# Optimization experiments

Measured on AMD Instinct MI355X. Metric: run time of the kernel, lower is better.

Reference implementation:

```python
import jax, jax.numpy as jnp
import numpy as np

# Module hyper-parameters (from create_with_implicit_mesh defaults)
KERNEL_RADIUS = 4
KERNEL_SIGMA2 = 0.5
EPS = 1e-8


def _forward_shift(src, flow):
    """Flow-based forward splatting with Gaussian-kernel scatter-add.

    Each source pixel at integer grid location (x, y) lands at the continuous
    target position p = (x + u, y + v). Its value is splatted onto all target
    pixels within KERNEL_RADIUS of p with weight exp(-||t - p||^2 / (2*sigma2)),
    accumulated atomically into weighted-image / weight / mask buffers.
    """
    B, C, H, W = src.shape
    HW = H * W
    R = KERNEL_RADIUS
    dt = src.dtype

    xs = jnp.arange(W, dtype=dt)
    ys = jnp.arange(H, dtype=dt)
    px = (xs[None, None, :] + flow[:, 0]).reshape(B, HW)   # continuous landing x
    py = (ys[None, :, None] + flow[:, 1]).reshape(B, HW)   # continuous landing y
    bx = jnp.floor(px).astype(jnp.int32)                   # base integer target
    by = jnp.floor(py).astype(jnp.int32)

    src_f = src.reshape(B, C, HW)
    acc_wI = jnp.zeros((B, C, HW), dt)
    acc_w = jnp.zeros((B, HW), dt)

    b2 = jnp.arange(B)[:, None]                 # (B,1) for (B,HW) scatter
    b3 = jnp.arange(B)[:, None, None]           # (B,1,1) for (B,C,HW) scatter
    c3 = jnp.arange(C)[None, :, None]           # (1,C,1)

    r2 = jnp.asarray(R * R, dt)
    for dy in range(-R, R + 1):
        for dx in range(-R, R + 1):
            tx = bx + dx
            ty = by + dy
            fx = tx.astype(dt)
            fy = ty.astype(dt)
            d2 = (fx - px) ** 2 + (fy - py) ** 2
            valid = (tx >= 0) & (tx < W) & (ty >= 0) & (ty < H) & (d2 <= r2)
            w = jnp.exp(-d2 / (2.0 * KERNEL_SIGMA2)) * valid.astype(dt)  # (B,HW)
            idx = jnp.clip(ty, 0, H - 1) * W + jnp.clip(tx, 0, W - 1)    # (B,HW)
            acc_w = acc_w.at[b2, idx].add(w)
            acc_wI = acc_wI.at[b3, c3, idx[:, None, :]].add(w[:, None, :] * src_f)

    w_img = acc_w.reshape(B, 1, H, W)
    out_img = acc_wI.reshape(B, C, H, W) / (w_img + EPS)
    mask = (w_img > 0).astype(dt)
    return out_img, mask


def setup_inputs() -> dict:
    key = jax.random.key(0)
    k1, k2 = jax.random.split(key)
    B, C, H, W = 4, 3, 720, 1280
    src_image = jax.random.normal(k1, (B, C, H, W), dtype=jnp.float32)
    flow_src_to_tar = jax.random.normal(k2, (B, 2, H, W), dtype=jnp.float32)
    return {"src_image": src_image, "flow_src_to_tar": flow_src_to_tar}


def reference(src_image, flow_src_to_tar):
    return _forward_shift(src_image, flow_src_to_tar)
```

## Files before the change

kernel.cpp:

```cpp
#include <hip/hip_runtime.h>
#include <hip/hip_fp16.h>

constexpr int B_N = 4;
constexpr int C_N = 3;
constexpr int H_IMG = 720;
constexpr int W_IMG = 1280;
constexpr int HW = H_IMG * W_IMG;

constexpr int TW = 64, TH = 32;
constexpr int HALO = 8;
constexpr int CW = TW + 2 * HALO;
constexpr int CH = TH + 2 * HALO;
constexpr int PITCH = CW + 1;
constexpr int PLANE = CH * PITCH;
constexpr float FLOW_MAX = 4.0f;
constexpr float LOG2E = 1.44269504f;

#define K1 0.36787944117144233f
#define K3 0.049787068367863944f
#define K5 0.006737946999085467f
#define K7 0.0009118819655545162f

typedef float v2f __attribute__((ext_vector_type(2)));
static __device__ __forceinline__ v2f splat2(float x) { return (v2f){x, x}; }

__global__ __launch_bounds__(256, 3)
void gather_kernel(const float* __restrict__ src, const float* __restrict__ flow,
                   float* __restrict__ out) {
    __shared__ __half2 UV[PLANE];
    __shared__ __half2 S01[PLANE];
    __shared__ float   S2[PLANE];

    const int b = blockIdx.z;
    const int tx0 = blockIdx.x * TW;
    const int ty0 = blockIdx.y * TH;
    const int cx0 = tx0 - HALO, cy0 = ty0 - HALO;

    const float* __restrict__ up = flow + (size_t)(b * 2) * HW;
    const float* __restrict__ vp = up + HW;
    const float* __restrict__ sp = src + (size_t)(b * 3) * HW;

    for (int idx = threadIdx.x; idx < CH * CW; idx += 256) {
        const int cy = idx / CW, cx = idx - cy * CW;
        const int gx = cx0 + cx, gy = cy0 + cy;
        float u = 300.f, v = 300.f, s0 = 0.f, s1 = 0.f, s2 = 0.f;
        if (gx >= 0 && gx < W_IMG && gy >= 0 && gy < H_IMG) {
            const int g = gy * W_IMG + gx;
            const float uu = up[g], vv = vp[g];
            if (fabsf(uu) <= FLOW_MAX && fabsf(vv) <= FLOW_MAX) {
                u = uu; v = vv;
                s0 = sp[g]; s1 = sp[HW + g]; s2 = sp[2 * HW + g];
            }
        }
        const int l = cy * PITCH + cx;
        UV[l] = __floats2half2_rn(u, v);
        S01[l] = __floats2half2_rn(s0, s1);
        S2[l] = s2;
    }
    __syncthreads();

    const int xg = threadIdx.x & 7;
    const int rL = threadIdx.x >> 3;
    const int ty = ty0 + rL;
    if (ty >= H_IMG) return;

    v2f AW[4], A0[4], A1[4], A2[4];
#pragma unroll
    for (int k = 0; k < 4; ++k) { AW[k] = splat2(0.f); A0[k] = splat2(0.f);
                                  A1[k] = splat2(0.f); A2[k] = splat2(0.f); }

    for (int oy = 0; oy < 17; ++oy) {
        const float Cy = (float)(oy - 8);
        const int rowbase = (rL + oy) * PITCH + 8 * xg;
#pragma unroll
        for (int ox = 0; ox < 24; ++ox) {
            const int l = rowbase + ox;
            const float2 uv = __half22float2(UV[l]);
            const float dx = uv.x + (float)(ox - 12);
            const float dy = uv.y + Cy;
            const float dxL = dx * LOG2E;
            const float tX = dx * dxL;
            const float dyL = dy * LOG2E;
            const float tY = dy * dyL;
            if (tX < 112.6f && tY < 36.2f) {
                const float E = __builtin_amdgcn_exp2f(-tX);
                const float g = dxL + dxL;
                const float G = __builtin_amdgcn_exp2f(g);
                const float Gi = __builtin_amdgcn_exp2f(-g);
                const float ey = __builtin_amdgcn_exp2f(-tY);

                const float m1 = G * K1, m3 = G * K3, m5 = G * K5;
                const float n1 = Gi * K1, n3 = Gi * K3, n5 = Gi * K5, n7 = Gi * K7;
                const float w4 = E;
                const float w5 = w4 * m1, w6 = w5 * m3, w7 = w6 * m5;
                const float w3 = w4 * n1, w2 = w3 * n3, w1 = w2 * n5, w0 = w1 * n7;

                const float2 s01 = __half22float2(S01[l]);
                const float s2v = S2[l];
                const v2f ey2 = splat2(ey);
                const v2f s0s = splat2(s01.x), s1s = splat2(s01.y), s2s = splat2(s2v);

                v2f W[4];
                W[0] = (v2f){w0, w1}; W[1] = (v2f){w2, w3};
                W[2] = (v2f){w4, w5}; W[3] = (v2f){w6, w7};
#pragma unroll
                for (int k = 0; k < 4; ++k) {
                    const v2f wt = W[k] * ey2;
                    AW[k] += wt;
                    A0[k] = __builtin_elementwise_fma(wt, s0s, A0[k]);
                    A1[k] = __builtin_elementwise_fma(wt, s1s, A1[k]);
                    A2[k] = __builtin_elementwise_fma(wt, s2s, A2[k]);
                }
            }
        }
    }

    float* __restrict__ wI = out;
    float* __restrict__ wb = out + (size_t)B_N * C_N * HW;
    const int tb = ty * W_IMG + tx0 + 8 * xg;
    float* p0 = wI + (size_t)(b * 3 + 0) * HW + tb;
    float* p1 = wI + (size_t)(b * 3 + 1) * HW + tb;
    float* p2 = wI + (size_t)(b * 3 + 2) * HW + tb;
    float* pw = wb + (size_t)b * HW + tb;
    *(float4*)(p0)     = make_float4(A0[0].x, A0[0].y, A0[1].x, A0[1].y);
    *(float4*)(p0 + 4) = make_float4(A0[2].x, A0[2].y, A0[3].x, A0[3].y);
    *(float4*)(p1)     = make_float4(A1[0].x, A1[0].y, A1[1].x, A1[1].y);
    *(float4*)(p1 + 4) = make_float4(A1[2].x, A1[2].y, A1[3].x, A1[3].y);
    *(float4*)(p2)     = make_float4(A2[0].x, A2[0].y, A2[1].x, A2[1].y);
    *(float4*)(p2 + 4) = make_float4(A2[2].x, A2[2].y, A2[3].x, A2[3].y);
    *(float4*)(pw)     = make_float4(AW[0].x, AW[0].y, AW[1].x, AW[1].y);
    *(float4*)(pw + 4) = make_float4(AW[2].x, AW[2].y, AW[3].x, AW[3].y);
}

__global__ __launch_bounds__(256)
void outlier_kernel(const float* __restrict__ src, const float* __restrict__ flow,
                    float* __restrict__ out) {
    const int i = blockIdx.x * 256 + threadIdx.x;
    if (i >= B_N * HW) return;
    const int b = i / HW, g = i - b * HW;
    const float* __restrict__ up = flow + (size_t)(b * 2) * HW;
    const float u = up[g], v = up[HW + g];
    if (fabsf(u) <= FLOW_MAX && fabsf(v) <= FLOW_MAX) return;

    const int x = g % W_IMG, y = g / W_IMG;
    const float px = (float)x + u, py = (float)y + v;
    if (!(px > -6.f && px < (float)W_IMG + 5.f &&
          py > -6.f && py < (float)H_IMG + 5.f)) return;

    const float bxf = floorf(px), byf = floorf(py);
    const int bx = (int)bxf, by = (int)byf;
    const float* __restrict__ sp = src + (size_t)(b * 3) * HW;
    const float s0 = sp[g], s1 = sp[HW + g], s2 = sp[2 * HW + g];
    float* __restrict__ wI = out;
    float* __restrict__ wb = out + (size_t)B_N * C_N * HW;

    for (int dyi = -4; dyi <= 4; ++dyi) {
        const int tyy = by + dyi;
        if (tyy < 0 || tyy >= H_IMG) continue;
        const float dyf = (byf + (float)dyi) - py;
        const float dy2 = dyf * dyf;
        for (int dxi = -4; dxi <= 4; ++dxi) {
            const int txx = bx + dxi;
            if (txx < 0 || txx >= W_IMG) continue;
            const float dxf = (bxf + (float)dxi) - px;
            const float d2 = fmaf(dxf, dxf, dy2);
            if (d2 > 16.f) continue;
            const float w = __expf(-d2);
            const int t = tyy * W_IMG + txx;
            atomicAdd(&wb[(size_t)b * HW + t], w);
            atomicAdd(&wI[(size_t)(b * 3 + 0) * HW + t], w * s0);
            atomicAdd(&wI[(size_t)(b * 3 + 1) * HW + t], w * s1);
            atomicAdd(&wI[(size_t)(b * 3 + 2) * HW + t], w * s2);
        }
    }
}

__global__ __launch_bounds__(256)
void finalize_kernel(float* __restrict__ out) {
    const int i = blockIdx.x * blockDim.x + threadIdx.x;
    const int n4 = B_N * HW / 4;
    if (i >= n4) return;
    const int per_b = HW / 4;
    const int b = i / per_b;
    const int hw = (i - b * per_b) * 4;
    float* __restrict__ wb = out + (size_t)B_N * C_N * HW + (size_t)b * HW + hw;
    float4 w = *(float4*)wb;
    const float4 inv = make_float4(1.f / (w.x + 1e-8f), 1.f / (w.y + 1e-8f),
                                   1.f / (w.z + 1e-8f), 1.f / (w.w + 1e-8f));
    float* base = out + (size_t)(b * 3) * HW + hw;
#pragma unroll
    for (int c = 0; c < 3; ++c) {
        float4 t = *(float4*)(base + (size_t)c * HW);
        t.x *= inv.x; t.y *= inv.y; t.z *= inv.z; t.w *= inv.w;
        *(float4*)(base + (size_t)c * HW) = t;
    }
    *(float4*)wb = make_float4(w.x > 0.f ? 1.f : 0.f, w.y > 0.f ? 1.f : 0.f,
                               w.z > 0.f ? 1.f : 0.f, w.w > 0.f ? 1.f : 0.f);
}

extern "C" void kernel_launch(void* const* d_in, const int* in_sizes, int n_in,
                              void* d_out, int out_size, void* d_ws, size_t ws_size,
                              hipStream_t stream) {
    const float* src = (const float*)d_in[0];
    const float* flow = (const float*)d_in[1];
    float* out = (float*)d_out;

    dim3 grid(W_IMG / TW, (H_IMG + TH - 1) / TH, B_N);
    gather_kernel<<<grid, 256, 0, stream>>>(src, flow, out);

    const int n = B_N * HW;
    outlier_kernel<<<(n + 255) / 256, 256, 0, stream>>>(src, flow, out);
    const int n4 = n / 4;
    finalize_kernel<<<(n4 + 255) / 256, 256, 0, stream>>>(out);
}
```

Baseline: 440.5 us.

## Register-block two output rows per thread, shrink halo, vectorize outlier scan

The gather kernel now computes two output rows per thread, deriving the second row's y-weight from the first by a recurrence. That shares the x-weight exp chain and LDS reads across both rows, and the branch on tX/tY is removed. The flow cutoff is lowered to 3.5 so the halo shrinks to 7 and the tile grows to 64x64, and the third source channel is stored in LDS as half precision to save shared memory. The outlier kernel reads four flow values per thread with a vector load and exits early when all four are inliers. The costs are more registers (occupancy hint lowered to 2), extra fp16 rounding error, and more pixels sent down the atomic outlier path.

```diff
diff --git a/kernel.cpp b/kernel.cpp
--- a/kernel.cpp
+++ b/kernel.cpp
@@ -7,29 +7,27 @@
 constexpr int W_IMG = 1280;
 constexpr int HW = H_IMG * W_IMG;
 
-constexpr int TW = 64, TH = 32;
-constexpr int HALO = 8;
+constexpr int TW = 64, TH = 64;
+constexpr int HALO = 7;
 constexpr int CW = TW + 2 * HALO;
 constexpr int CH = TH + 2 * HALO;
-constexpr int PITCH = CW + 1;
+constexpr int PITCH = 79;
 constexpr int PLANE = CH * PITCH;
-constexpr float FLOW_MAX = 4.0f;
+constexpr float FLOW_MAX = 3.5f;
 constexpr float LOG2E = 1.44269504f;
+constexpr float MARKER = 30.0f;
 
 #define K1 0.36787944117144233f
 #define K3 0.049787068367863944f
 #define K5 0.006737946999085467f
 #define K7 0.0009118819655545162f
 
-typedef float v2f __attribute__((ext_vector_type(2)));
-static __device__ __forceinline__ v2f splat2(float x) { return (v2f){x, x}; }
-
-__global__ __launch_bounds__(256, 3)
+__global__ __launch_bounds__(256, 2)
 void gather_kernel(const float* __restrict__ src, const float* __restrict__ flow,
                    float* __restrict__ out) {
     __shared__ __half2 UV[PLANE];
     __shared__ __half2 S01[PLANE];
-    __shared__ float   S2[PLANE];
+    __shared__ __half  S2[PLANE];
 
     const int b = blockIdx.z;
     const int tx0 = blockIdx.x * TW;
@@ -41,9 +39,9 @@
     const float* __restrict__ sp = src + (size_t)(b * 3) * HW;
 
     for (int idx = threadIdx.x; idx < CH * CW; idx += 256) {
-        const int cy = idx / CW, cx = idx - cy * CW;
-        const int gx = cx0 + cx, gy = cy0 + cy;
-        float u = 300.f, v = 300.f, s0 = 0.f, s1 = 0.f, s2 = 0.f;
+        const int cr = idx / CW, cx = idx - cr * CW;
+        const int gx = cx0 + cx, gy = cy0 + cr;
+        float u = MARKER, v = MARKER, s0 = 0.f, s1 = 0.f, s2 = 0.f;
         if (gx >= 0 && gx < W_IMG && gy >= 0 && gy < H_IMG) {
             const int g = gy * W_IMG + gx;
             const float uu = up[g], vv = vp[g];
@@ -52,125 +50,153 @@
                 s0 = sp[g]; s1 = sp[HW + g]; s2 = sp[2 * HW + g];
             }
         }
-        const int l = cy * PITCH + cx;
+        const int l = cr * PITCH + cx;
         UV[l] = __floats2half2_rn(u, v);
         S01[l] = __floats2half2_rn(s0, s1);
-        S2[l] = s2;
+        S2[l] = __float2half_rn(s2);
     }
     __syncthreads();
 
     const int xg = threadIdx.x & 7;
-    const int rL = threadIdx.x >> 3;
-    const int ty = ty0 + rL;
-    if (ty >= H_IMG) return;
-
-    v2f AW[4], A0[4], A1[4], A2[4];
-#pragma unroll
-    for (int k = 0; k < 4; ++k) { AW[k] = splat2(0.f); A0[k] = splat2(0.f);
-                                  A1[k] = splat2(0.f); A2[k] = splat2(0.f); }
-
-    for (int oy = 0; oy < 17; ++oy) {
-        const float Cy = (float)(oy - 8);
-        const int rowbase = (rL + oy) * PITCH + 8 * xg;
-#pragma unroll
-        for (int ox = 0; ox < 24; ++ox) {
-            const int l = rowbase + ox;
+    const int yg = threadIdx.x >> 3;
+    const int ty_a = ty0 + 2 * yg;
+
+    float aW[2][8], a0[2][8], a1[2][8], a2[2][8];
+#pragma unroll
+    for (int j = 0; j < 2; ++j)
+#pragma unroll
+        for (int i = 0; i < 8; ++i) { aW[j][i] = 0.f; a0[j][i] = 0.f;
+                                      a1[j][i] = 0.f; a2[j][i] = 0.f; }
+
+    for (int oy = 0; oy < 16; ++oy) {
+        const float Cy = (float)(oy - 7);
+        const int lrow = (2 * yg + oy) * PITCH + 8 * xg;
+#pragma unroll
+        for (int ox = 0; ox < 22; ++ox) {
+            const int l = lrow + ox;
             const float2 uv = __half22float2(UV[l]);
-            const float dx = uv.x + (float)(ox - 12);
+            const float2 s01 = __half22float2(S01[l]);
+            const float s2v = __half2float(S2[l]);
+
+            const float dx = uv.x + (float)(ox - 11);
             const float dy = uv.y + Cy;
-            const float dxL = dx * LOG2E;
-            const float tX = dx * dxL;
-            const float dyL = dy * LOG2E;
-            const float tY = dy * dyL;
-            if (tX < 112.6f && tY < 36.2f) {
-                const float E = __builtin_amdgcn_exp2f(-tX);
-                const float g = dxL + dxL;
-                const float G = __builtin_amdgcn_exp2f(g);
-                const float Gi = __builtin_amdgcn_exp2f(-g);
-                const float ey = __builtin_amdgcn_exp2f(-tY);
-
-                const float m1 = G * K1, m3 = G * K3, m5 = G * K5;
-                const float n1 = Gi * K1, n3 = Gi * K3, n5 = Gi * K5, n7 = Gi * K7;
-                const float w4 = E;
-                const float w5 = w4 * m1, w6 = w5 * m3, w7 = w6 * m5;
-                const float w3 = w4 * n1, w2 = w3 * n3, w1 = w2 * n5, w0 = w1 * n7;
-
-                const float2 s01 = __half22float2(S01[l]);
-                const float s2v = S2[l];
-                const v2f ey2 = splat2(ey);
-                const v2f s0s = splat2(s01.x), s1s = splat2(s01.y), s2s = splat2(s2v);
-
-                v2f W[4];
-                W[0] = (v2f){w0, w1}; W[1] = (v2f){w2, w3};
-                W[2] = (v2f){w4, w5}; W[3] = (v2f){w6, w7};
-#pragma unroll
-                for (int k = 0; k < 4; ++k) {
-                    const v2f wt = W[k] * ey2;
-                    AW[k] += wt;
-                    A0[k] = __builtin_elementwise_fma(wt, s0s, A0[k]);
-                    A1[k] = __builtin_elementwise_fma(wt, s1s, A1[k]);
-                    A2[k] = __builtin_elementwise_fma(wt, s2s, A2[k]);
-                }
+
+            const float aL = dx * LOG2E;
+            const float tX = aL * dx;
+            const float E  = __builtin_amdgcn_exp2f(-tX);
+            const float g  = aL + aL;
+            const float G  = __builtin_amdgcn_exp2f(g);
+            const float Gi = __builtin_amdgcn_exp2f(-g);
+
+            const float bL = dy * LOG2E;
+            const float tY = bL * dy;
+            const float eya = __builtin_amdgcn_exp2f(-tY);
+            const float gy = bL + bL;
+            const float Gy = __builtin_amdgcn_exp2f(gy);
+            const float rk = Gy * K1;
+
+            const float m1 = G * K1, m3 = G * K3, m5 = G * K5;
+            const float n1 = Gi * K1, n3 = Gi * K3, n5 = Gi * K5, n7 = Gi * K7;
+            float w[8];
+            w[4] = E;
+            w[5] = w[4] * m1; w[6] = w[5] * m3; w[7] = w[6] * m5;
+            w[3] = w[4] * n1; w[2] = w[3] * n3; w[1] = w[2] * n5; w[0] = w[1] * n7;
+
+            const float zw0 = eya,        zw1 = eya * rk;
+            const float z00 = s01.x * eya, z01 = z00 * rk;
+            const float z10 = s01.y * eya, z11 = z10 * rk;
+            const float z20 = s2v * eya,   z21 = z20 * rk;
+
+#pragma unroll
+            for (int i = 0; i < 8; ++i) {
+                aW[0][i] = fmaf(w[i], zw0, aW[0][i]);
+                aW[1][i] = fmaf(w[i], zw1, aW[1][i]);
+                a0[0][i] = fmaf(w[i], z00, a0[0][i]);
+                a0[1][i] = fmaf(w[i], z01, a0[1][i]);
+                a1[0][i] = fmaf(w[i], z10, a1[0][i]);
+                a1[1][i] = fmaf(w[i], z11, a1[1][i]);
+                a2[0][i] = fmaf(w[i], z20, a2[0][i]);
+                a2[1][i] = fmaf(w[i], z21, a2[1][i]);
             }
         }
     }
 
     float* __restrict__ wI = out;
     float* __restrict__ wb = out + (size_t)B_N * C_N * HW;
-    const int tb = ty * W_IMG + tx0 + 8 * xg;
-    float* p0 = wI + (size_t)(b * 3 + 0) * HW + tb;
-    float* p1 = wI + (size_t)(b * 3 + 1) * HW + tb;
-    float* p2 = wI + (size_t)(b * 3 + 2) * HW + tb;
-    float* pw = wb + (size_t)b * HW + tb;
-    *(float4*)(p0)     = make_float4(A0[0].x, A0[0].y, A0[1].x, A0[1].y);
-    *(float4*)(p0 + 4) = make_float4(A0[2].x, A0[2].y, A0[3].x, A0[3].y);
-    *(float4*)(p1)     = make_float4(A1[0].x, A1[0].y, A1[1].x, A1[1].y);
-    *(float4*)(p1 + 4) = make_float4(A1[2].x, A1[2].y, A1[3].x, A1[3].y);
-    *(float4*)(p2)     = make_float4(A2[0].x, A2[0].y, A2[1].x, A2[1].y);
-    *(float4*)(p2 + 4) = make_float4(A2[2].x, A2[2].y, A2[3].x, A2[3].y);
-    *(float4*)(pw)     = make_float4(AW[0].x, AW[0].y, AW[1].x, AW[1].y);
-    *(float4*)(pw + 4) = make_float4(AW[2].x, AW[2].y, AW[3].x, AW[3].y);
+    const int gx0 = tx0 + 8 * xg;
+#pragma unroll
+    for (int j = 0; j < 2; ++j) {
+        const int ty = ty_a + j;
+        if (ty >= H_IMG) continue;
+        const int tb = ty * W_IMG + gx0;
+        float* p0 = wI + (size_t)(b * 3 + 0) * HW + tb;
+        float* p1 = wI + (size_t)(b * 3 + 1) * HW + tb;
+        float* p2 = wI + (size_t)(b * 3 + 2) * HW + tb;
+        float* pw = wb + (size_t)b * HW + tb;
+        *(float4*)(p0)     = make_float4(a0[j][0], a0[j][1], a0[j][2], a0[j][3]);
+        *(float4*)(p0 + 4) = make_float4(a0[j][4], a0[j][5], a0[j][6], a0[j][7]);
+        *(float4*)(p1)     = make_float4(a1[j][0], a1[j][1], a1[j][2], a1[j][3]);
+        *(float4*)(p1 + 4) = make_float4(a1[j][4], a1[j][5], a1[j][6], a1[j][7]);
+        *(float4*)(p2)     = make_float4(a2[j][0], a2[j][1], a2[j][2], a2[j][3]);
+        *(float4*)(p2 + 4) = make_float4(a2[j][4], a2[j][5], a2[j][6], a2[j][7]);
+        *(float4*)(pw)     = make_float4(aW[j][0], aW[j][1], aW[j][2], aW[j][3]);
+        *(float4*)(pw + 4) = make_float4(aW[j][4], aW[j][5], aW[j][6], aW[j][7]);
+    }
 }
 
 __global__ __launch_bounds__(256)
 void outlier_kernel(const float* __restrict__ src, const float* __restrict__ flow,
                     float* __restrict__ out) {
-    const int i = blockIdx.x * 256 + threadIdx.x;
-    if (i >= B_N * HW) return;
-    const int b = i / HW, g = i - b * HW;
+    const int n4 = B_N * HW / 4;
+    const int i4 = blockIdx.x * 256 + threadIdx.x;
+    if (i4 >= n4) return;
+    const int per_b = HW / 4;
+    const int b = i4 / per_b;
+    const int g0 = (i4 - b * per_b) * 4;
     const float* __restrict__ up = flow + (size_t)(b * 2) * HW;
-    const float u = up[g], v = up[HW + g];
-    if (fabsf(u) <= FLOW_MAX && fabsf(v) <= FLOW_MAX) return;
-
-    const int x = g % W_IMG, y = g / W_IMG;
-    const float px = (float)x + u, py = (float)y + v;
-    if (!(px > -6.f && px < (float)W_IMG + 5.f &&
-          py > -6.f && py < (float)H_IMG + 5.f)) return;
-
-    const float bxf = floorf(px), byf = floorf(py);
-    const int bx = (int)bxf, by = (int)byf;
+    const float4 u4 = *(const float4*)(up + g0);
+    const float4 v4 = *(const float4*)(up + HW + g0);
+    const float um = fmaxf(fmaxf(fabsf(u4.x), fabsf(u4.y)), fmaxf(fabsf(u4.z), fabsf(u4.w)));
+    const float vm = fmaxf(fmaxf(fabsf(v4.x), fabsf(v4.y)), fmaxf(fabsf(v4.z), fabsf(v4.w)));
+    if (um <= FLOW_MAX && vm <= FLOW_MAX) return;
+
+    const float uu[4] = {u4.x, u4.y, u4.z, u4.w};
+    const float vv[4] = {v4.x, v4.y, v4.z, v4.w};
     const float* __restrict__ sp = src + (size_t)(b * 3) * HW;
-    const float s0 = sp[g], s1 = sp[HW + g], s2 = sp[2 * HW + g];
     float* __restrict__ wI = out;
     float* __restrict__ wb = out + (size_t)B_N * C_N * HW;
 
-    for (int dyi = -4; dyi <= 4; ++dyi) {
-        const int tyy = by + dyi;
-        if (tyy < 0 || tyy >= H_IMG) continue;
-        const float dyf = (byf + (float)dyi) - py;
-        const float dy2 = dyf * dyf;
-        for (int dxi = -4; dxi <= 4; ++dxi) {
-            const int txx = bx + dxi;
-            if (txx < 0 || txx >= W_IMG) continue;
-            const float dxf = (bxf + (float)dxi) - px;
-            const float d2 = fmaf(dxf, dxf, dy2);
-            if (d2 > 16.f) continue;
-            const float w = __expf(-d2);
-            const int t = tyy * W_IMG + txx;
-            atomicAdd(&wb[(size_t)b * HW + t], w);
-            atomicAdd(&wI[(size_t)(b * 3 + 0) * HW + t], w * s0);
-            atomicAdd(&wI[(size_t)(b * 3 + 1) * HW + t], w * s1);
-            atomicAdd(&wI[(size_t)(b * 3 + 2) * HW + t], w * s2);
+    for (int k = 0; k < 4; ++k) {
+        const float u = uu[k], v = vv[k];
+        if (fabsf(u) <= FLOW_MAX && fabsf(v) <= FLOW_MAX) continue;
+        const int g = g0 + k;
+        const int x = g % W_IMG, y = g / W_IMG;
+        const float px = (float)x + u, py = (float)y + v;
+        if (!(px > -6.f && px < (float)W_IMG + 5.f &&
+              py > -6.f && py < (float)H_IMG + 5.f)) continue;
+
+        const float bxf = floorf(px), byf = floorf(py);
+        const int bx = (int)bxf, by = (int)byf;
+        const float s0 = sp[g], s1 = sp[HW + g], s2 = sp[2 * HW + g];
+
+        for (int dyi = -4; dyi <= 4; ++dyi) {
+            const int tyy = by + dyi;
+            if (tyy < 0 || tyy >= H_IMG) continue;
+            const float dyf = (byf + (float)dyi) - py;
+            const float dy2 = dyf * dyf;
+            for (int dxi = -4; dxi <= 4; ++dxi) {
+                const int txx = bx + dxi;
+                if (txx < 0 || txx >= W_IMG) continue;
+                const float dxf = (bxf + (float)dxi) - px;
+                const float d2 = fmaf(dxf, dxf, dy2);
+                if (d2 > 16.f) continue;
+                const float w = __expf(-d2);
+                const int t = tyy * W_IMG + txx;
+                atomicAdd(&wb[(size_t)b * HW + t], w);
+                atomicAdd(&wI[(size_t)(b * 3 + 0) * HW + t], w * s0);
+                atomicAdd(&wI[(size_t)(b * 3 + 1) * HW + t], w * s1);
+                atomicAdd(&wI[(size_t)(b * 3 + 2) * HW + t], w * s2);
+            }
         }
     }
 }
@@ -208,8 +234,7 @@
     dim3 grid(W_IMG / TW, (H_IMG + TH - 1) / TH, B_N);
     gather_kernel<<<grid, 256, 0, stream>>>(src, flow, out);
 
-    const int n = B_N * HW;
-    outlier_kernel<<<(n + 255) / 256, 256, 0, stream>>>(src, flow, out);
-    const int n4 = n / 4;
+    const int n4 = B_N * HW / 4;
+    outlier_kernel<<<(n4 + 255) / 256, 256, 0, stream>>>(src, flow, out);
     finalize_kernel<<<(n4 + 255) / 256, 256, 0, stream>>>(out);
 }
```

Measured after the change: 442.0 us. Within noise of the previous version (+0.3%).
